# Kernel tuning notes

Hardware: AMD Instinct MI355X
Metric: run time of the kernel (lower is better)

## Reference

```python
import jax, jax.numpy as jnp
import numpy as np

# ---- placement DB constants (from init_kwargs) ----
XL, XH, YL, YH = 0.0, 1000.0, 0.0, 1000.0
NBX, NBY = 256, 256
BSX = (XH - XL) / NBX
BSY = (YH - YL) / NBY
UHC, UVC = 1.5625, 1.45           # unit horizontal/vertical routing capacity
MAX_RATE = 2.0
MIN_RATE = 1.0 / MAX_RATE
NUM_NETS = 100000
NUM_NODES = 120000
NUM_MOVABLE = 100000
PINS_PER_NET = 4
NUM_PINS = NUM_NETS * PINS_PER_NET


def setup_inputs() -> dict:
    key = jax.random.key(0)
    k1, k2, k3, k4, k5, k6 = jax.random.split(key, 6)
    # node positions: x block then y block, kept inside the die
    pos_x = jax.random.uniform(k1, (NUM_NODES,), jnp.float32) * (XH - XL - 5.0) + XL
    pos_y = jax.random.uniform(k2, (NUM_NODES,), jnp.float32) * (YH - YL - 5.0) + YL
    pos = jnp.concatenate([pos_x, pos_y])
    # pin positions: x block then y block
    pin_x = jax.random.uniform(k3, (NUM_PINS,), jnp.float32) * (XH - XL) + XL
    pin_y = jax.random.uniform(k4, (NUM_PINS,), jnp.float32) * (YH - YL) + YL
    pin_pos = jnp.concatenate([pin_x, pin_y])
    # node sizes in [1, 5)
    node_size_x = jax.random.uniform(k5, (NUM_NODES,), jnp.float32) * 4.0 + 1.0
    node_size_y = jax.random.uniform(k6, (NUM_NODES,), jnp.float32) * 4.0 + 1.0
    net_weights = jnp.ones((NUM_NETS,), jnp.float32)
    # ragged net->pin CSR: fixed 4 pins per net, randomly permuted pin ids
    netpin_start = jnp.arange(NUM_NETS + 1, dtype=jnp.int64) * PINS_PER_NET
    flat_netpin = jax.random.permutation(jax.random.key(7), NUM_PINS).astype(jnp.int64)
    return {"pos": pos, "pin_pos": pin_pos, "node_size_x": node_size_x,
            "node_size_y": node_size_y, "net_weights": net_weights,
            "netpin_start": netpin_start, "flat_netpin": flat_netpin}


def _overlap_1d(lo, hi, nbins, bl, bs):
    """Overlap length of [lo,hi] intervals with each bin. lo,hi: [N] -> [N, nbins]."""
    bin_lo = bl + bs * jnp.arange(nbins, dtype=lo.dtype)
    bin_hi = bin_lo + bs
    ov = jnp.minimum(hi[:, None], bin_hi[None, :]) - jnp.maximum(lo[:, None], bin_lo[None, :])
    return jnp.maximum(ov, 0.0)


def reference(pos, pin_pos, node_size_x, node_size_y, net_weights, netpin_start, flat_netpin):
    num_pins = pin_pos.shape[0] // 2
    # ---- phase 1: per-net bbox via ragged CSR gather + segment reduce ----
    px = pin_pos[flat_netpin]             # [P] pin x
    py = pin_pos[flat_netpin + num_pins]  # [P] pin y
    seg = jnp.searchsorted(netpin_start[1:], jnp.arange(flat_netpin.shape[0]), side='right')
    xmin = jax.ops.segment_min(px, seg, num_segments=NUM_NETS)
    xmax = jax.ops.segment_max(px, seg, num_segments=NUM_NETS)
    ymin = jax.ops.segment_min(py, seg, num_segments=NUM_NETS)
    ymax = jax.ops.segment_max(py, seg, num_segments=NUM_NETS)
    wx = xmax - xmin
    wy = ymax - ymin
    bbox_area = jnp.maximum(wx * wy, jnp.float32(1e-6))  # guard degenerate nets
    # RUDY demand densities (per unit area inside the bbox)
    h_dens = net_weights * wx / bbox_area  # horizontal demand density
    v_dens = net_weights * wy / bbox_area  # vertical demand density
    # separable bbox-bin overlaps
    ox = _overlap_1d(xmin, xmax, NBX, XL, BSX)  # [N, Bx]
    oy = _overlap_1d(ymin, ymax, NBY, YL, BSY)  # [N, By]
    h_map = jnp.einsum('nx,ny->xy', ox * h_dens[:, None], oy)  # [Bx, By]
    v_map = jnp.einsum('nx,ny->xy', ox * v_dens[:, None], oy)
    h_util = h_map / (BSX * BSY * UHC)
    v_util = v_map / (BSX * BSY * UVC)
    util = jnp.clip(jnp.maximum(h_util, v_util), MIN_RATE, MAX_RATE)
    # ---- phase 2: scatter congestion-weighted area to movable nodes ----
    nx = pos[:NUM_MOVABLE]
    ny = pos[NUM_NODES:NUM_NODES + NUM_MOVABLE]
    sx = node_size_x[:NUM_MOVABLE]
    sy = node_size_y[:NUM_MOVABLE]
    oxn = _overlap_1d(nx, nx + sx, NBX, XL, BSX)  # [M, Bx]
    oyn = _overlap_1d(ny, ny + sy, NBY, YL, BSY)  # [M, By]
    instance_route_area = jnp.einsum('ix,xy,iy->i', oxn, util, oyn)  # [M]
    return instance_route_area
```

## Files before the change

kernel.cpp:

```cpp
#include <hip/hip_runtime.h>


#define NB 256
#define NW 4
#define NWIN 64
#define NCHUNK 16
#define K2_THREADS 512
#define FXS 65536.0f
#define INV_FXS (1.0f / 65536.0f)
#define LCAP 1000
#define LFLUSH 488

__device__ __forceinline__ long long load_idx(const void* p, long long i, int is64) {
    if (is64) return ((const long long*)p)[i];
    return (long long)((const int*)p)[i];
}

__global__ void bbox_kernel(const float* __restrict__ pin_pos,
                            const float* __restrict__ net_weights,
                            const void* __restrict__ netpin_start,
                            const void* __restrict__ flat_netpin,
                            unsigned long long* __restrict__ wmask,
                            float2* __restrict__ yb,
                            float4* __restrict__ rd,
                            int num_nets, int num_pins) {
    int gid = blockIdx.x * blockDim.x + threadIdx.x;
    int n = gid >> 2, k = gid & 3;
    if (n >= num_nets) return;
    const int is64 = (((const int*)netpin_start)[1] == 0);
    long long s = load_idx(netpin_start, n, is64);
    long long e = load_idx(netpin_start, n + 1, is64);
    float xmn = 3e38f, xmx = -3e38f, ymn = 3e38f, ymx = -3e38f;
    if (e - s == 4) {
        long long pin = load_idx(flat_netpin, s + k, is64);
        float px = pin_pos[pin], py = pin_pos[pin + num_pins];
        xmn = px; xmx = px; ymn = py; ymx = py;
    } else if (k == 0) {
        for (long long p = s; p < e; ++p) {
            long long pin = load_idx(flat_netpin, p, is64);
            float px = pin_pos[pin], py = pin_pos[pin + num_pins];
            xmn = fminf(xmn, px); xmx = fmaxf(xmx, px);
            ymn = fminf(ymn, py); ymx = fmaxf(ymx, py);
        }
    }
    #pragma unroll
    for (int m = 1; m <= 2; m <<= 1) {
        xmn = fminf(xmn, __shfl_xor(xmn, m));
        xmx = fmaxf(xmx, __shfl_xor(xmx, m));
        ymn = fminf(ymn, __shfl_xor(ymn, m));
        ymx = fmaxf(ymx, __shfl_xor(ymx, m));
    }
    if (k) return;
    if (e <= s) { wmask[n] = 0ull; return; }
    float wx = xmx - xmn, wy = ymx - ymn;
    float area = fmaxf(wx * wy, 1e-6f);
    float w = net_weights[n];
    const float INVB = 1.0f / 3.90625f;
    int j0 = (int)floorf(ymn * INVB);
    int j1 = (int)floorf(ymx * INVB);
    unsigned long long m = 0ull;
    if ((unsigned)j0 < 256u)       m |= 1ull << (j0 >> 2);
    if ((unsigned)(j0 + 1) < 256u) m |= 1ull << ((j0 + 1) >> 2);
    if ((unsigned)j1 < 256u)       m |= 1ull << (j1 >> 2);
    if ((unsigned)(j1 + 1) < 256u) m |= 1ull << ((j1 + 1) >> 2);
    wmask[n] = m;
    yb[n] = make_float2(ymn, ymx);
    rd[n] = make_float4(xmn, xmx, w * wx / area, w * wy / area);
}

__global__ __launch_bounds__(K2_THREADS) void accum8(
        const unsigned long long* __restrict__ wmask,
        const float2* __restrict__ yb,
        const float4* __restrict__ rd,
        float* __restrict__ PT,
        int num_nets) {
    __shared__ float acc[2 * NW * NB];
    __shared__ float l_y0[LCAP], l_y1[LCAP], l_x0[LCAP], l_x1[LCAP];
    __shared__ float l_dh[LCAP], l_dv[LCAP];
    __shared__ int   lcount;
    int* acci = (int*)acc;
    const int win   = blockIdx.x >> 4;
    const int chunk = blockIdx.x & 15;
    const int r0    = win * NW;
    const int tid   = threadIdx.x;
    const int lane  = tid & 63;
    const float BSX  = 3.90625f;
    const float INVB = 1.0f / 3.90625f;

    for (int i = tid; i < 2 * NW * NB; i += K2_THREADS) acci[i] = 0;
    if (tid == 0) lcount = 0;
    __syncthreads();

    const int c0 = (int)((long long)num_nets * chunk / NCHUNK);
    const int c1 = (int)((long long)num_nets * (chunk + 1) / NCHUNK);
    const int nstrips = (c1 - c0 + K2_THREADS - 1) / K2_THREADS;

    for (int s = 0; s < nstrips; ++s) {
        int n = c0 + s * K2_THREADS + tid;
        bool hit = (n < c1) && ((wmask[n] >> win) & 1ull);
        float2 y; float4 r;
        if (hit) { y = yb[n]; r = rd[n]; }
        unsigned long long m = __ballot(hit);
        if (m) {
            int base = 0;
            if (lane == 0) base = atomicAdd(&lcount, (int)__popcll(m));
            base = __shfl(base, 0);
            if (hit) {
                int pos = base + (int)__popcll(m & ((1ull << lane) - 1ull));
                l_y0[pos] = y.x; l_y1[pos] = y.y;
                l_x0[pos] = r.x; l_x1[pos] = r.y;
                l_dh[pos] = r.z; l_dv[pos] = r.w;
            }
        }
        __syncthreads();
        int cnt = lcount;
        if (cnt >= LFLUSH || s == nstrips - 1) {
            for (int i = tid; i < cnt; i += K2_THREADS) {
                float ty0 = l_y0[i] * INVB, fj0 = floorf(ty0);
                float ty1 = l_y1[i] * INVB, fj1 = floorf(ty1);
                int j0 = (int)fj0, j1 = (int)fj1;
                float f0 = ty0 - fj0, f1 = ty1 - fj1;
                float tx0 = l_x0[i] * INVB, g0 = floorf(tx0);
                float tx1 = l_x1[i] * INVB, g1 = floorf(tx1);
                int i0 = (int)g0, i1 = (int)g1;
                float h0 = tx0 - g0, h1 = tx1 - g1;
                float dh = l_dh[i], dv = l_dv[i];
                int   xx[4] = { i0, i0 + 1, i1, i1 + 1 };
                float ax[4] = { BSX * (1.f - h0), BSX * h0,
                               -BSX * (1.f - h1), -BSX * h1 };
                int   rr[4] = { j0, j0 + 1, j1, j1 + 1 };
                float rw[4] = { BSX * (1.f - f0), BSX * f0,
                               -BSX * (1.f - f1), -BSX * f1 };
                #pragma unroll
                for (int q = 0; q < 4; ++q) {
                    int ro = rr[q] - r0;
                    if ((unsigned)ro >= NW) continue;
                    float wh = rw[q] * dh * FXS;
                    float wv = rw[q] * dv * FXS;
                    int* bh = acci + ro * NB;
                    int* bv = acci + NW * NB + ro * NB;
                    #pragma unroll
                    for (int p = 0; p < 4; ++p) {
                        int x = xx[p];
                        if (x >= NB) continue;
                        atomicAdd(bh + x, __float2int_rn(ax[p] * wh));
                        atomicAdd(bv + x, __float2int_rn(ax[p] * wv));
                    }
                }
            }
            __syncthreads();
            if (tid == 0) lcount = 0;
            __syncthreads();
        }
    }

    const int wave = tid >> 6;
    for (int row = wave; row < 2 * NW; row += (K2_THREADS / 64)) {
        float carry = 0.f;
        #pragma unroll
        for (int seg = 0; seg < NB / 64; ++seg) {
            int idx = row * NB + seg * 64 + lane;
            float v = (float)acci[idx] * INV_FXS;
            #pragma unroll
            for (int off = 1; off < 64; off <<= 1) {
                float u = __shfl_up(v, off);
                if (lane >= off) v += u;
            }
            v += carry;
            acc[idx] = v;
            carry = __shfl(v, 63);
        }
    }
    __syncthreads();

    {
        int i = tid;
        int p = i >> 8;
        int x = i & 255;
        int base = p * NW * NB;
        float4 v;
        v.x = acc[base + 0 * NB + x];
        v.y = acc[base + 1 * NB + x];
        v.z = acc[base + 2 * NB + x];
        v.w = acc[base + 3 * NB + x];
        float* dst = PT + ((((long long)chunk * 2 + p) * NB + x) * NB) + r0;
        *(float4*)dst = v;
    }
}

__global__ __launch_bounds__(512) void yscan_util(
        const float* __restrict__ PT, float* __restrict__ utilT) {
    __shared__ float buf[2 * NB];
    const int x = blockIdx.x;
    const int plane = threadIdx.x >> 8;
    const int y = threadIdx.x & (NB - 1);
    float s = 0.f;
    #pragma unroll 8
    for (int c = 0; c < NCHUNK; ++c)
        s += PT[(((long long)c * 2 + plane) * NB + x) * NB + y];
    float* b = buf + plane * NB;
    b[y] = s;
    #pragma unroll
    for (int off = 1; off < NB; off <<= 1) {
        __syncthreads();
        float a = (y >= off) ? b[y - off] : 0.0f;
        __syncthreads();
        b[y] += a;
    }
    __syncthreads();
    if (plane == 0) {
        const float INV_CH = 1.0f / (3.90625f * 3.90625f * 1.5625f);
        const float INV_CV = 1.0f / (3.90625f * 3.90625f * 1.45f);
        float u = fmaxf(buf[y] * INV_CH, buf[NB + y] * INV_CV);
        u = fminf(fmaxf(u, 0.5f), 2.0f);
        utilT[x * NB + y] = u;
    }
}

__global__ void instance_area(const float* __restrict__ pos,
                              const float* __restrict__ nsx,
                              const float* __restrict__ nsy,
                              const float* __restrict__ utilT,
                              float* __restrict__ out,
                              int num_movable, int num_nodes) {
    int i = blockIdx.x * blockDim.x + threadIdx.x;
    if (i >= num_movable) return;
    const float BSX = 3.90625f;
    const float INVB = 1.0f / 3.90625f;
    float x0f = pos[i];
    float y0f = pos[num_nodes + i];
    float x1f = x0f + nsx[i];
    float y1f = y0f + nsy[i];
    int kx0 = max(0, min(NB - 1, (int)floorf(x0f * INVB)));
    int kx1 = max(0, min(NB - 1, (int)floorf(x1f * INVB)));
    int ky0 = max(0, min(NB - 1, (int)floorf(y0f * INVB)));
    int ky1 = max(0, min(NB - 1, (int)floorf(y1f * INVB)));
    float acc = 0.0f;
    for (int kx = kx0; kx <= kx1; ++kx) {
        float bx = kx * BSX;
        float ovx = fmaxf(fminf(x1f, bx + BSX) - fmaxf(x0f, bx), 0.0f);
        const float* ucol = utilT + kx * NB;
        float accy = 0.0f;
        for (int ky = ky0; ky <= ky1; ++ky) {
            float by = ky * BSX;
            float ovy = fmaxf(fminf(y1f, by + BSX) - fmaxf(y0f, by), 0.0f);
            accy += ovy * ucol[ky];
        }
        acc += accy * ovx;
    }
    out[i] = acc;
}

__global__ void fb_zero(float* g, int n) {
    int i = blockIdx.x * blockDim.x + threadIdx.x;
    int stride = gridDim.x * blockDim.x;
    for (; i < n; i += stride) g[i] = 0.0f;
}

__global__ void fb_scatter(const float* __restrict__ pin_pos,
                           const float* __restrict__ net_weights,
                           const void* __restrict__ netpin_start,
                           const void* __restrict__ flat_netpin,
                           float* __restrict__ G2,
                           int num_nets, int num_pins) {
    int n = blockIdx.x * blockDim.x + threadIdx.x;
    if (n >= num_nets) return;
    const int is64 = (((const int*)netpin_start)[1] == 0);
    long long s = load_idx(netpin_start, n, is64);
    long long e = load_idx(netpin_start, n + 1, is64);
    if (e <= s) return;
    float xmn = 3e38f, xmx = -3e38f, ymn = 3e38f, ymx = -3e38f;
    for (long long p = s; p < e; ++p) {
        long long pin = load_idx(flat_netpin, p, is64);
        float px = pin_pos[pin], py = pin_pos[pin + num_pins];
        xmn = fminf(xmn, px); xmx = fmaxf(xmx, px);
        ymn = fminf(ymn, py); ymx = fmaxf(ymx, py);
    }
    float wx = xmx - xmn, wy = ymx - ymn;
    float area = fmaxf(wx * wy, 1e-6f);
    float w = net_weights[n];
    float dh = w * wx / area, dv = w * wy / area;
    const float BSX = 3.90625f, INVB = 1.0f / 3.90625f;
    int jx[4]; float ax[4]; int jy[4]; float ay[4];
    float t, fj, f; int j;
    t = xmn * INVB; fj = floorf(t); j = (int)fj; f = t - fj;
    jx[0] = j; ax[0] = BSX * (1.f - f); jx[1] = j + 1; ax[1] = BSX * f;
    t = xmx * INVB; fj = floorf(t); j = (int)fj; f = t - fj;
    jx[2] = j; ax[2] = -BSX * (1.f - f); jx[3] = j + 1; ax[3] = -BSX * f;
    t = ymn * INVB; fj = floorf(t); j = (int)fj; f = t - fj;
    jy[0] = j; ay[0] = BSX * (1.f - f); jy[1] = j + 1; ay[1] = BSX * f;
    t = ymx * INVB; fj = floorf(t); j = (int)fj; f = t - fj;
    jy[2] = j; ay[2] = -BSX * (1.f - f); jy[3] = j + 1; ay[3] = -BSX * f;
    #pragma unroll
    for (int b = 0; b < 4; ++b) {
        int y = jy[b];
        if (y < 0 || y >= NB) continue;
        #pragma unroll
        for (int a2 = 0; a2 < 4; ++a2) {
            int x = jx[a2];
            if (x < 0 || x >= NB) continue;
            float g = ax[a2] * ay[b];
            atomicAdd(&G2[(y * NB + x) * 2],     dh * g);
            atomicAdd(&G2[(y * NB + x) * 2 + 1], dv * g);
        }
    }
}

__global__ void fb_rowscan(float2* G2) {
    int y = blockIdx.x, t = threadIdx.x;
    __shared__ float sh[NB]; __shared__ float sv[NB];
    float2 v = G2[y * NB + t];
    sh[t] = v.x; sv[t] = v.y;
    #pragma unroll
    for (int off = 1; off < NB; off <<= 1) {
        __syncthreads();
        float a = (t >= off) ? sh[t - off] : 0.0f;
        float b = (t >= off) ? sv[t - off] : 0.0f;
        __syncthreads();
        sh[t] += a; sv[t] += b;
    }
    __syncthreads();
    G2[y * NB + t] = make_float2(sh[t], sv[t]);
}

__global__ void fb_colscan(const float2* __restrict__ G2, float* __restrict__ utilT) {
    int x = blockIdx.x, t = threadIdx.x;
    const float INV_CH = 1.0f / (3.90625f * 3.90625f * 1.5625f);
    const float INV_CV = 1.0f / (3.90625f * 3.90625f * 1.45f);
    __shared__ float sh[NB]; __shared__ float sv[NB];
    float2 g = G2[t * NB + x];
    sh[t] = g.x; sv[t] = g.y;
    #pragma unroll
    for (int off = 1; off < NB; off <<= 1) {
        __syncthreads();
        float a = (t >= off) ? sh[t - off] : 0.0f;
        float b = (t >= off) ? sv[t - off] : 0.0f;
        __syncthreads();
        sh[t] += a; sv[t] += b;
    }
    __syncthreads();
    float u = fmaxf(sh[t] * INV_CH, sv[t] * INV_CV);
    utilT[x * NB + t] = fminf(fmaxf(u, 0.5f), 2.0f);
}

extern "C" void kernel_launch(void* const* d_in, const int* in_sizes, int n_in,
                              void* d_out, int out_size, void* d_ws, size_t ws_size,
                              hipStream_t stream) {
    const float* pos          = (const float*)d_in[0];
    const float* pin_pos      = (const float*)d_in[1];
    const float* nsx          = (const float*)d_in[2];
    const float* nsy          = (const float*)d_in[3];
    const float* net_weights  = (const float*)d_in[4];
    const void*  netpin_start = d_in[5];
    const void*  flat_netpin  = d_in[6];
    float* out = (float*)d_out;

    int num_pins    = in_sizes[1] / 2;
    int num_nodes   = in_sizes[2];
    int num_nets    = in_sizes[4];
    int num_movable = out_size;

    auto align4 = [](size_t v) { return (v + 3) & ~(size_t)3; };
    size_t mk_off = 0;
    size_t yb_off = align4(mk_off + 2LL * num_nets);
    size_t rd_off = align4(yb_off + 2LL * num_nets);
    size_t PT_off = align4(rd_off + 4LL * num_nets);
    size_t PT_f   = (size_t)NCHUNK * 2 * NB * NB;
    size_t ut_off = PT_off + PT_f;
    size_t need   = (ut_off + (size_t)NB * NB) * sizeof(float);

    if (ws_size >= need) {
        float* base = (float*)d_ws;
        unsigned long long* wmask = (unsigned long long*)(base + mk_off);
        float2*   yb    = (float2*)(base + yb_off);
        float4*   rd    = (float4*)(base + rd_off);
        float*    PT    = base + PT_off;
        float*    ut    = base + ut_off;

        int g1 = (4 * num_nets + 255) / 256;
        bbox_kernel<<<g1, 256, 0, stream>>>(pin_pos, net_weights, netpin_start,
                                            flat_netpin, wmask, yb, rd,
                                            num_nets, num_pins);
        accum8<<<NWIN * NCHUNK, K2_THREADS, 0, stream>>>(wmask, yb, rd, PT, num_nets);
        yscan_util<<<NB, 512, 0, stream>>>(PT, ut);
        int gi = (num_movable + 255) / 256;
        instance_area<<<gi, 256, 0, stream>>>(pos, nsx, nsy, ut, out,
                                              num_movable, num_nodes);
        return;
    }

    {
        float* G2   = (float*)d_ws;
        float* util = G2 + NB * NB * 2;
        fb_zero<<<256, 256, 0, stream>>>(G2, NB * NB * 2);
        int gn = (num_nets + 255) / 256;
        fb_scatter<<<gn, 256, 0, stream>>>(pin_pos, net_weights, netpin_start,
                                           flat_netpin, G2, num_nets, num_pins);
        fb_rowscan<<<NB, 256, 0, stream>>>((float2*)G2);
        fb_colscan<<<NB, 256, 0, stream>>>((const float2*)G2, util);
        int gi = (num_movable + 255) / 256;
        instance_area<<<gi, 256, 0, stream>>>(pos, nsx, nsy, util, out,
                                              num_movable, num_nodes);
    }
}
```

Before: 39.33 us.

## Prefetch window masks into registers and defer per-strip barriers in accumulation

The accumulation kernel now loads every strip's window mask into registers up front and stores only net indices in LDS. yb/rd are gathered from global memory at flush time, and the per-strip __syncthreads is gone, so barriers happen only when the list reaches a larger flush threshold or at the last strip. The aim is fewer block-wide barriers, less LDS traffic and footprint, and memory loads issued early. The trade-offs are extra registers for the mask array and an unsynchronized read of lcount that decides the flush branch, which could diverge across waves or drop entries past the capacity guard if hit counts were high. The fast path is also gated on the strip count fitting MAXSTRIPS.

```diff
diff --git a/kernel.cpp b/kernel.cpp
--- a/kernel.cpp
+++ b/kernel.cpp
@@ -8,8 +8,9 @@
 #define K2_THREADS 512
 #define FXS 65536.0f
 #define INV_FXS (1.0f / 65536.0f)
-#define LCAP 1000
-#define LFLUSH 488
+#define LCAP 2048
+#define LFLUSH 1536
+#define MAXSTRIPS 16
 
 __device__ __forceinline__ long long load_idx(const void* p, long long i, int is64) {
     if (is64) return ((const long long*)p)[i];
@@ -68,15 +69,14 @@
     rd[n] = make_float4(xmn, xmx, w * wx / area, w * wy / area);
 }
 
-__global__ __launch_bounds__(K2_THREADS) void accum8(
+__global__ __launch_bounds__(K2_THREADS) void accum9(
         const unsigned long long* __restrict__ wmask,
         const float2* __restrict__ yb,
         const float4* __restrict__ rd,
         float* __restrict__ PT,
         int num_nets) {
     __shared__ float acc[2 * NW * NB];
-    __shared__ float l_y0[LCAP], l_y1[LCAP], l_x0[LCAP], l_x1[LCAP];
-    __shared__ float l_dh[LCAP], l_dv[LCAP];
+    __shared__ int   l_idx[LCAP];
     __shared__ int   lcount;
     int* acci = (int*)acc;
     const int win   = blockIdx.x >> 4;
@@ -89,17 +89,60 @@
 
     for (int i = tid; i < 2 * NW * NB; i += K2_THREADS) acci[i] = 0;
     if (tid == 0) lcount = 0;
-    __syncthreads();
 
     const int c0 = (int)((long long)num_nets * chunk / NCHUNK);
     const int c1 = (int)((long long)num_nets * (chunk + 1) / NCHUNK);
     const int nstrips = (c1 - c0 + K2_THREADS - 1) / K2_THREADS;
 
+    unsigned long long wm[MAXSTRIPS];
+    #pragma unroll
+    for (int s = 0; s < MAXSTRIPS; ++s) {
+        int n = c0 + s * K2_THREADS + tid;
+        wm[s] = (s < nstrips && n < c1) ? wmask[n] : 0ull;
+    }
+    __syncthreads();
+
+    auto flush = [&](int cnt) {
+        for (int i = tid; i < cnt; i += K2_THREADS) {
+            int n = l_idx[i];
+            float2 y = yb[n];
+            float4 r = rd[n];
+            float ty0 = y.x * INVB, fj0 = floorf(ty0);
+            float ty1 = y.y * INVB, fj1 = floorf(ty1);
+            int j0 = (int)fj0, j1 = (int)fj1;
+            float f0 = ty0 - fj0, f1 = ty1 - fj1;
+            float tx0 = r.x * INVB, g0 = floorf(tx0);
+            float tx1 = r.y * INVB, g1 = floorf(tx1);
+            int i0 = (int)g0, i1 = (int)g1;
+            float h0 = tx0 - g0, h1 = tx1 - g1;
+            int   xx[4] = { i0, i0 + 1, i1, i1 + 1 };
+            float ax[4] = { BSX * (1.f - h0), BSX * h0,
+                           -BSX * (1.f - h1), -BSX * h1 };
+            int   rr[4] = { j0, j0 + 1, j1, j1 + 1 };
+            float rw[4] = { BSX * (1.f - f0), BSX * f0,
+                           -BSX * (1.f - f1), -BSX * f1 };
+            #pragma unroll
+            for (int q = 0; q < 4; ++q) {
+                int ro = rr[q] - r0;
+                if ((unsigned)ro >= NW) continue;
+                float wh = rw[q] * r.z * FXS;
+                float wv = rw[q] * r.w * FXS;
+                int* bh = acci + ro * NB;
+                int* bv = acci + NW * NB + ro * NB;
+                #pragma unroll
+                for (int p = 0; p < 4; ++p) {
+                    int x = xx[p];
+                    if (x >= NB) continue;
+                    atomicAdd(bh + x, __float2int_rn(ax[p] * wh));
+                    atomicAdd(bv + x, __float2int_rn(ax[p] * wv));
+                }
+            }
+        }
+    };
+
     for (int s = 0; s < nstrips; ++s) {
         int n = c0 + s * K2_THREADS + tid;
-        bool hit = (n < c1) && ((wmask[n] >> win) & 1ull);
-        float2 y; float4 r;
-        if (hit) { y = yb[n]; r = rd[n]; }
+        bool hit = ((wm[s] >> win) & 1ull) != 0ull;
         unsigned long long m = __ballot(hit);
         if (m) {
             int base = 0;
@@ -107,47 +150,13 @@
             base = __shfl(base, 0);
             if (hit) {
                 int pos = base + (int)__popcll(m & ((1ull << lane) - 1ull));
-                l_y0[pos] = y.x; l_y1[pos] = y.y;
-                l_x0[pos] = r.x; l_x1[pos] = r.y;
-                l_dh[pos] = r.z; l_dv[pos] = r.w;
+                if (pos < LCAP) l_idx[pos] = n;
             }
         }
-        __syncthreads();
-        int cnt = lcount;
-        if (cnt >= LFLUSH || s == nstrips - 1) {
-            for (int i = tid; i < cnt; i += K2_THREADS) {
-                float ty0 = l_y0[i] * INVB, fj0 = floorf(ty0);
-                float ty1 = l_y1[i] * INVB, fj1 = floorf(ty1);
-                int j0 = (int)fj0, j1 = (int)fj1;
-                float f0 = ty0 - fj0, f1 = ty1 - fj1;
-                float tx0 = l_x0[i] * INVB, g0 = floorf(tx0);
-                float tx1 = l_x1[i] * INVB, g1 = floorf(tx1);
-                int i0 = (int)g0, i1 = (int)g1;
-                float h0 = tx0 - g0, h1 = tx1 - g1;
-                float dh = l_dh[i], dv = l_dv[i];
-                int   xx[4] = { i0, i0 + 1, i1, i1 + 1 };
-                float ax[4] = { BSX * (1.f - h0), BSX * h0,
-                               -BSX * (1.f - h1), -BSX * h1 };
-                int   rr[4] = { j0, j0 + 1, j1, j1 + 1 };
-                float rw[4] = { BSX * (1.f - f0), BSX * f0,
-                               -BSX * (1.f - f1), -BSX * f1 };
-                #pragma unroll
-                for (int q = 0; q < 4; ++q) {
-                    int ro = rr[q] - r0;
-                    if ((unsigned)ro >= NW) continue;
-                    float wh = rw[q] * dh * FXS;
-                    float wv = rw[q] * dv * FXS;
-                    int* bh = acci + ro * NB;
-                    int* bv = acci + NW * NB + ro * NB;
-                    #pragma unroll
-                    for (int p = 0; p < 4; ++p) {
-                        int x = xx[p];
-                        if (x >= NB) continue;
-                        atomicAdd(bh + x, __float2int_rn(ax[p] * wh));
-                        atomicAdd(bv + x, __float2int_rn(ax[p] * wv));
-                    }
-                }
-            }
+        if (s == nstrips - 1 || lcount >= LFLUSH) {
+            __syncthreads();
+            int cnt = lcount; if (cnt > LCAP) cnt = LCAP;
+            flush(cnt);
             __syncthreads();
             if (tid == 0) lcount = 0;
             __syncthreads();
@@ -369,7 +378,10 @@
     size_t ut_off = PT_off + PT_f;
     size_t need   = (ut_off + (size_t)NB * NB) * sizeof(float);
 
-    if (ws_size >= need) {
+    bool strips_ok = ((num_nets + NCHUNK - 1) / NCHUNK + K2_THREADS - 1) / K2_THREADS
+                     <= MAXSTRIPS;
+
+    if (ws_size >= need && strips_ok) {
         float* base = (float*)d_ws;
         unsigned long long* wmask = (unsigned long long*)(base + mk_off);
         float2*   yb    = (float2*)(base + yb_off);
@@ -381,7 +393,7 @@
         bbox_kernel<<<g1, 256, 0, stream>>>(pin_pos, net_weights, netpin_start,
                                             flat_netpin, wmask, yb, rd,
                                             num_nets, num_pins);
-        accum8<<<NWIN * NCHUNK, K2_THREADS, 0, stream>>>(wmask, yb, rd, PT, num_nets);
+        accum9<<<NWIN * NCHUNK, K2_THREADS, 0, stream>>>(wmask, yb, rd, PT, num_nets);
         yscan_util<<<NB, 512, 0, stream>>>(PT, ut);
         int gi = (num_movable + 255) / 256;
         instance_area<<<gi, 256, 0, stream>>>(pos, nsx, nsy, ut, out,
```

Result: faster. 35.72 us (-9.2%).
